# Performance work log

Hardware: AMD Instinct MI355X
Metric: run time of the kernel (lower is better)

The kernel has to match this reference:

```python
import jax, jax.numpy as jnp
import numpy as np

H_S = 1024
N_HEADS = 16
P_S = H_S // N_HEADS
LN_EPS = 1e-5


def layer_norm(x, gamma, beta):
    mu = jnp.mean(x, axis=-1, keepdims=True)
    var = jnp.var(x, axis=-1, keepdims=True)
    return (x - mu) * jax.lax.rsqrt(var + LN_EPS) * gamma + beta


def setup_inputs() -> dict:
    key = jax.random.key(0)
    ks = jax.random.split(key, 8)
    scale = 1.0 / np.sqrt(H_S)
    B, S = 4, 2048
    return {
        "q": jax.random.normal(ks[0], (B, S, H_S), jnp.float32),
        "k": jax.random.normal(ks[1], (B, S, H_S), jnp.float32),
        "v": jax.random.normal(ks[2], (B, S, H_S), jnp.float32),
        "ln_q_g": jnp.ones((H_S,), jnp.float32),
        "ln_q_b": jnp.zeros((H_S,), jnp.float32),
        "ln_k_g": jnp.ones((H_S,), jnp.float32),
        "ln_k_b": jnp.zeros((H_S,), jnp.float32),
        "ln_v_g": jnp.ones((H_S,), jnp.float32),
        "ln_v_b": jnp.zeros((H_S,), jnp.float32),
        "w_q": jax.random.normal(ks[3], (H_S, H_S), jnp.float32) * scale,
        "w_k": jax.random.normal(ks[4], (H_S, H_S), jnp.float32) * scale,
        "w_v": jax.random.normal(ks[5], (H_S, H_S), jnp.float32) * scale,
        "w_fc": jax.random.normal(ks[6], (H_S, H_S), jnp.float32) * scale,
        "b_fc": jnp.zeros((H_S,), jnp.float32),
    }


def _split_heads(x):
    # (b, s, h_s) -> (b, n_heads, s, p_s)
    b, s, _ = x.shape
    return x.reshape(b, s, N_HEADS, P_S).transpose(0, 2, 1, 3)


def reference(q, k, v, ln_q_g, ln_q_b, ln_k_g, ln_k_b, ln_v_g, ln_v_b,
              w_q, w_k, w_v, w_fc, b_fc):
    b, q_l, _ = q.shape
    # LayerNorm + Linear (bias=False) for Q/K/V, then head split
    qh = _split_heads(layer_norm(q, ln_q_g, ln_q_b) @ w_q.T)
    kh = _split_heads(layer_norm(k, ln_k_g, ln_k_b) @ w_k.T)
    vh = _split_heads(layer_norm(v, ln_v_g, ln_v_b) @ w_v.T)
    # scaled dot-product attention (clipping_distance=None path), scale 1/sqrt(p_s)
    scores = jnp.einsum("bhqp,bhkp->bhqk", qh, kh) / jnp.sqrt(jnp.float32(P_S))
    attn = jax.nn.softmax(scores, axis=-1)
    ctx = jnp.einsum("bhqk,bhkp->bhqp", attn, vh)
    # join heads: (b, h, q, p) -> (b, q, h_s)
    ctx = ctx.transpose(0, 2, 1, 3).reshape(b, q_l, H_S)
    out = ctx @ w_fc.T + b_fc
    # residual (dropout p=0.0 -> identity)
    return q + out
```

## Files before the change

kernel.cpp:

```cpp
#include <hip/hip_runtime.h>

#define HS 1024
#define NH 16
#define PS 64
#define SS 2048
#define NB 4
#define MTOT (NB * SS)
#define QSCALE 0.18033688011112042f

typedef __bf16 bf16x8 __attribute__((ext_vector_type(8)));
typedef float f32x4 __attribute__((ext_vector_type(4)));

__device__ __forceinline__ unsigned short f2bf(float f) {
  union { __bf16 h; unsigned short u; } c;
  c.h = (__bf16)f;
  return c.u;
}
__device__ __forceinline__ unsigned int pk2(float a, float b) {
  union { __bf16 h[2]; unsigned int u; } c;
  c.h[0] = (__bf16)a; c.h[1] = (__bf16)b;
  return c.u;
}
__device__ __forceinline__ float exp2x(float x) {
  float r; asm("v_exp_f32 %0, %1" : "=v"(r) : "v"(x)); return r;
}
__device__ __forceinline__ int kp32(int k) {
  return (k & ~31) | ((k & 12) << 1) | ((k & 16) >> 2) | (k & 3);
}

__device__ __forceinline__ void gload16(const void* g, void* lds) {
  __builtin_amdgcn_global_load_lds(
      (const __attribute__((address_space(1))) unsigned int*)g,
      (__attribute__((address_space(3))) unsigned int*)lds, 16, 0, 0);
}

__device__ __forceinline__ bf16x8 ldfrag128(const unsigned short* base, int r, int c) {
  union { bf16x8 v; uint4 u; } f;
  f.u = *reinterpret_cast<const uint4*>(base + r * 64 + ((c ^ (r & 7)) << 3));
  return f.v;
}

__global__ __launch_bounds__(256) void ln3_kernel(
    const float* __restrict__ x0, const float* __restrict__ x1, const float* __restrict__ x2,
    const float* __restrict__ g0, const float* __restrict__ b0,
    const float* __restrict__ g1, const float* __restrict__ b1,
    const float* __restrict__ g2, const float* __restrict__ b2,
    unsigned short* __restrict__ y0, unsigned short* __restrict__ y1,
    unsigned short* __restrict__ y2) {
  const int z = blockIdx.y;
  const float* x = z == 0 ? x0 : z == 1 ? x1 : x2;
  const float* g = z == 0 ? g0 : z == 1 ? g1 : g2;
  const float* bt = z == 0 ? b0 : z == 1 ? b1 : b2;
  unsigned short* y = z == 0 ? y0 : z == 1 ? y1 : y2;
  const int row = blockIdx.x;
  const int t = threadIdx.x;
  const float4 v = reinterpret_cast<const float4*>(x + (size_t)row * HS)[t];
  float s = v.x + v.y + v.z + v.w;
  float s2 = v.x * v.x + v.y * v.y + v.z * v.z + v.w * v.w;
#pragma unroll
  for (int m = 32; m; m >>= 1) { s += __shfl_xor(s, m); s2 += __shfl_xor(s2, m); }
  __shared__ float red[8];
  if ((t & 63) == 0) { red[t >> 6] = s; red[4 + (t >> 6)] = s2; }
  __syncthreads();
  s = red[0] + red[1] + red[2] + red[3];
  s2 = red[4] + red[5] + red[6] + red[7];
  const float mean = s * (1.0f / HS);
  const float var = s2 * (1.0f / HS) - mean * mean;
  const float rs = rsqrtf(var + 1e-5f);
  const float4 gv = reinterpret_cast<const float4*>(g)[t];
  const float4 bv = reinterpret_cast<const float4*>(bt)[t];
  uint2 o;
  o.x = pk2((v.x - mean) * rs * gv.x + bv.x, (v.y - mean) * rs * gv.y + bv.y);
  o.y = pk2((v.z - mean) * rs * gv.z + bv.z, (v.w - mean) * rs * gv.w + bv.w);
  *reinterpret_cast<uint2*>(y + (size_t)row * HS + kp32(4 * t)) = o;
}

__global__ __launch_bounds__(256) void castw_kernel(
    const float* __restrict__ w0, const float* __restrict__ w1,
    const float* __restrict__ w2, const float* __restrict__ w3,
    unsigned short* __restrict__ o0, unsigned short* __restrict__ o1,
    unsigned short* __restrict__ o2, unsigned short* __restrict__ o3) {
  const int which = blockIdx.x >> 10;
  const float* w = which == 0 ? w0 : which == 1 ? w1 : which == 2 ? w2 : w3;
  unsigned short* o = which == 0 ? o0 : which == 1 ? o1 : which == 2 ? o2 : o3;
  const int i = (blockIdx.x & 1023) * 256 + threadIdx.x;
  float4 v = reinterpret_cast<const float4*>(w)[i];
  uint2 u;
  u.x = pk2(v.x, v.y);
  u.y = pk2(v.z, v.w);
  *reinterpret_cast<uint2*>(o + (size_t)(i >> 8) * 1024 + kp32((i << 2) & 1023)) = u;
}

__global__ __launch_bounds__(512, 4) void gemm_qkv(
    const unsigned short* __restrict__ Aq, const unsigned short* __restrict__ Ak,
    const unsigned short* __restrict__ Av, const unsigned short* __restrict__ Wq,
    const unsigned short* __restrict__ Wk, const unsigned short* __restrict__ Wv,
    unsigned short* __restrict__ Pq, unsigned short* __restrict__ Pk,
    unsigned short* __restrict__ Pv, int zbase) {
  const int z = zbase + blockIdx.z;
  const unsigned short* A = z == 0 ? Aq : z == 1 ? Ak : Av;
  const unsigned short* Bw = z == 0 ? Wq : z == 1 ? Wk : Wv;
  unsigned short* out = z == 0 ? Pq : z == 1 ? Pk : Pv;
  __shared__ unsigned short As[128 * 64];
  __shared__ unsigned short Bs[128 * 64];
  const int t = threadIdx.x;
  const int id = blockIdx.x + 8 * blockIdx.y;
  const int xcd = id & 7, j = id >> 3;
  const int colT = (j & 7) * 128;
  const int rowT = (xcd * 8 + (j >> 3)) * 128;
  const int lane = t & 63;
  const int w = t >> 6;
  const int wr = (w >> 2) * 64, wc = (w & 3) * 32;
  const int c16 = lane & 15, g = lane >> 4, g4 = g << 2;
  const unsigned short* Ab = A + (size_t)rowT * 1024;
  const unsigned short* Bb = Bw + (size_t)colT * 1024;
  f32x4 acc[4][2] = {};
  for (int kt = 0; kt < 1024; kt += 64) {
#pragma unroll
    for (int i = 0; i < 2; ++i) {
      const int c = i * 512 + t;
      const int col = kt + (((c ^ (c >> 3)) & 7) << 3);
      gload16(Ab + (size_t)(c >> 3) * 1024 + col, As + c * 8);
      gload16(Bb + (size_t)(c >> 3) * 1024 + col, Bs + c * 8);
    }
    __syncthreads();
#pragma unroll
    for (int kk = 0; kk < 2; ++kk) {
      bf16x8 aF[4], bF[2];
#pragma unroll
      for (int m = 0; m < 4; ++m) aF[m] = ldfrag128(As, wr + m * 16 + c16, kk * 4 + g);
#pragma unroll
      for (int n = 0; n < 2; ++n) bF[n] = ldfrag128(Bs, wc + n * 16 + c16, kk * 4 + g);
      __builtin_amdgcn_s_setprio(1);
#pragma unroll
      for (int m = 0; m < 4; ++m)
#pragma unroll
        for (int n = 0; n < 2; ++n)
          acc[m][n] = __builtin_amdgcn_mfma_f32_16x16x32_bf16(aF[m], bF[n], acc[m][n], 0, 0, 0);
      __builtin_amdgcn_s_setprio(0);
    }
    __syncthreads();
  }
  const float sc = (z == 0) ? QSCALE : 1.0f;
#pragma unroll
  for (int m = 0; m < 4; ++m) {
#pragma unroll
    for (int n = 0; n < 2; ++n) {
#pragma unroll
      for (int r = 0; r < 4; ++r) {
        const int row = rowT + wr + m * 16 + g4 + r;
        const int col = colT + wc + n * 16 + c16;
        const float val = acc[m][n][r] * sc;
        const int b = row >> 11, s = row & 2047, h = col >> 6, p = col & 63;
        if (z == 2) {
          out[(((size_t)(b * NH + h)) * PS + p) * SS + kp32(s)] = f2bf(val);
        } else {
          out[(((size_t)(b * NH + h)) * SS + s) * PS + kp32(p)] = f2bf(val);
        }
      }
    }
  }
}

__global__ __launch_bounds__(512, 4) void gemm_fc(
    const unsigned short* __restrict__ A, const unsigned short* __restrict__ Bw,
    float* __restrict__ out, const float* __restrict__ resid,
    const float* __restrict__ bias) {
  __shared__ unsigned short As[128 * 64];
  __shared__ unsigned short Bs[128 * 64];
  const int t = threadIdx.x;
  const int id = blockIdx.x + 8 * blockIdx.y;
  const int xcd = id & 7, j = id >> 3;
  const int colT = (j & 7) * 128;
  const int rowT = (xcd * 8 + (j >> 3)) * 128;
  const int lane = t & 63;
  const int w = t >> 6;
  const int wr = (w >> 2) * 64, wc = (w & 3) * 32;
  const int c16 = lane & 15, g = lane >> 4, g4 = g << 2;
  const unsigned short* Ab = A + (size_t)rowT * 1024;
  const unsigned short* Bb = Bw + (size_t)colT * 1024;
  f32x4 acc[4][2] = {};
  for (int kt = 0; kt < 1024; kt += 64) {
#pragma unroll
    for (int i = 0; i < 2; ++i) {
      const int c = i * 512 + t;
      const int col = kt + (((c ^ (c >> 3)) & 7) << 3);
      gload16(Ab + (size_t)(c >> 3) * 1024 + col, As + c * 8);
      gload16(Bb + (size_t)(c >> 3) * 1024 + col, Bs + c * 8);
    }
    __syncthreads();
#pragma unroll
    for (int kk = 0; kk < 2; ++kk) {
      bf16x8 aF[4], bF[2];
#pragma unroll
      for (int m = 0; m < 4; ++m) aF[m] = ldfrag128(As, wr + m * 16 + c16, kk * 4 + g);
#pragma unroll
      for (int n = 0; n < 2; ++n) bF[n] = ldfrag128(Bs, wc + n * 16 + c16, kk * 4 + g);
      __builtin_amdgcn_s_setprio(1);
#pragma unroll
      for (int m = 0; m < 4; ++m)
#pragma unroll
        for (int n = 0; n < 2; ++n)
          acc[m][n] = __builtin_amdgcn_mfma_f32_16x16x32_bf16(aF[m], bF[n], acc[m][n], 0, 0, 0);
      __builtin_amdgcn_s_setprio(0);
    }
    __syncthreads();
  }
#pragma unroll
  for (int m = 0; m < 4; ++m) {
#pragma unroll
    for (int n = 0; n < 2; ++n) {
#pragma unroll
      for (int r = 0; r < 4; ++r) {
        const int row = rowT + wr + m * 16 + g4 + r;
        const int col = colT + wc + n * 16 + c16;
        out[(size_t)row * HS + col] =
            acc[m][n][r] + bias[col] + resid[(size_t)row * HS + col];
      }
    }
  }
}

__device__ __forceinline__ void stage_kv128(const unsigned short* Kb,
                                            const unsigned short* Vb, int tile,
                                            unsigned short* kd, unsigned short* vd,
                                            int t) {
#pragma unroll
  for (int i = 0; i < 2; ++i) {
    const int c = i * 512 + t;
    const int rk = c >> 3;
    const int ck = ((c ^ rk) & 7) << 3;
    gload16(Kb + (size_t)(tile * 128 + rk) * PS + ck, kd + c * 8);
    const int cc = c & 511;
    const int rv = cc >> 3;
    const int cv = ((cc ^ rv) & 7) << 3;
    gload16(Vb + (size_t)rv * SS + tile * 128 + i * 64 + cv, vd + c * 8);
  }
}

__global__ __launch_bounds__(512, 4) void attn_kernel(
    const unsigned short* __restrict__ Qp, const unsigned short* __restrict__ Kp,
    const unsigned short* __restrict__ Vtg, unsigned short* __restrict__ ctx) {
  __shared__ unsigned short Ks[2][128 * 64];
  __shared__ unsigned short Vs[2][128 * 64];
  const int t = threadIdx.x;
  const int w = t >> 6, lane = t & 63;
  const int c16 = lane & 15, g = lane >> 4, g4 = g << 2;
  const int id = blockIdx.x + 8 * blockIdx.y;
  const int xcd = id & 7, j = id >> 3;
  const int bh = xcd * 8 + (j >> 3);
  const int qbase = (j & 7) * 256 + w * 32;
  const unsigned short* Qb = Qp + (size_t)bh * SS * PS;
  const unsigned short* Kb = Kp + (size_t)bh * SS * PS;
  const unsigned short* Vb = Vtg + (size_t)bh * SS * PS;

  union { bf16x8 v; unsigned short s[8]; } ou;
#pragma unroll
  for (int i = 0; i < 8; ++i) ou.s[i] = 0x3F80;
  const bf16x8 onesv = ou.v;

  bf16x8 qF0[2], qF1[2];
#pragma unroll
  for (int kkc = 0; kkc < 2; ++kkc) {
    union { bf16x8 v; uint4 u; } f0, f1;
    f0.u = *reinterpret_cast<const uint4*>(Qb + (size_t)(qbase + c16) * PS + ((kkc * 4 + g) << 3));
    f1.u = *reinterpret_cast<const uint4*>(Qb + (size_t)(qbase + 16 + c16) * PS + ((kkc * 4 + g) << 3));
    qF0[kkc] = f0.v; qF1[kkc] = f1.v;
  }
  f32x4 o0[4] = {}, o1[4] = {};
  f32x4 ol0 = {}, ol1 = {};

  stage_kv128(Kb, Vb, 0, Ks[0], Vs[0], t);

  int buf = 0;
  for (int kt = 0; kt < 16; ++kt) {
    asm volatile("s_waitcnt vmcnt(0) lgkmcnt(0)" ::: "memory");
    __builtin_amdgcn_s_barrier();
    __builtin_amdgcn_sched_barrier(0);
    if (kt + 1 < 16) stage_kv128(Kb, Vb, kt + 1, Ks[buf ^ 1], Vs[buf ^ 1], t);

#pragma unroll
    for (int hh = 0; hh < 2; ++hh) {
      const unsigned short* kh = &Ks[buf][hh * 4096];
      const unsigned short* vh = &Vs[buf][hh * 4096];

      f32x4 s0[4] = {}, s1[4] = {};
      __builtin_amdgcn_s_setprio(1);
#pragma unroll
      for (int kkc = 0; kkc < 2; ++kkc)
#pragma unroll
        for (int nf = 0; nf < 4; ++nf) {
          const bf16x8 kf = ldfrag128(kh, nf * 16 + c16, kkc * 4 + g);
          s0[nf] = __builtin_amdgcn_mfma_f32_16x16x32_bf16(kf, qF0[kkc], s0[nf], 0, 0, 0);
          s1[nf] = __builtin_amdgcn_mfma_f32_16x16x32_bf16(kf, qF1[kkc], s1[nf], 0, 0, 0);
        }
      __builtin_amdgcn_s_setprio(0);

#pragma unroll
      for (int nf = 0; nf < 4; ++nf)
#pragma unroll
        for (int r = 0; r < 4; ++r) {
          s0[nf][r] = exp2x(s0[nf][r]);
          s1[nf][r] = exp2x(s1[nf][r]);
        }

      __builtin_amdgcn_s_setprio(1);
#pragma unroll
      for (int kkc = 0; kkc < 2; ++kkc) {
        union { bf16x8 v; unsigned int u[4]; } pa0, pa1;
        pa0.u[0] = pk2(s0[2 * kkc][0], s0[2 * kkc][1]);
        pa0.u[1] = pk2(s0[2 * kkc][2], s0[2 * kkc][3]);
        pa0.u[2] = pk2(s0[2 * kkc + 1][0], s0[2 * kkc + 1][1]);
        pa0.u[3] = pk2(s0[2 * kkc + 1][2], s0[2 * kkc + 1][3]);
        pa1.u[0] = pk2(s1[2 * kkc][0], s1[2 * kkc][1]);
        pa1.u[1] = pk2(s1[2 * kkc][2], s1[2 * kkc][3]);
        pa1.u[2] = pk2(s1[2 * kkc + 1][0], s1[2 * kkc + 1][1]);
        pa1.u[3] = pk2(s1[2 * kkc + 1][2], s1[2 * kkc + 1][3]);
        ol0 = __builtin_amdgcn_mfma_f32_16x16x32_bf16(pa0.v, onesv, ol0, 0, 0, 0);
        ol1 = __builtin_amdgcn_mfma_f32_16x16x32_bf16(pa1.v, onesv, ol1, 0, 0, 0);
#pragma unroll
        for (int pf = 0; pf < 4; ++pf) {
          const bf16x8 vf = ldfrag128(vh, pf * 16 + c16, kkc * 4 + g);
          o0[pf] = __builtin_amdgcn_mfma_f32_16x16x32_bf16(pa0.v, vf, o0[pf], 0, 0, 0);
          o1[pf] = __builtin_amdgcn_mfma_f32_16x16x32_bf16(pa1.v, vf, o1[pf], 0, 0, 0);
        }
      }
      __builtin_amdgcn_s_setprio(0);
    }

    buf ^= 1;
  }

  float i0[4], i1[4];
#pragma unroll
  for (int r = 0; r < 4; ++r) { i0[r] = 1.0f / ol0[r]; i1[r] = 1.0f / ol1[r]; }
  const int b = bh >> 4, h = bh & 15;
#pragma unroll
  for (int pf = 0; pf < 4; ++pf) {
#pragma unroll
    for (int r = 0; r < 4; ++r) {
      const int col = kp32(h * PS + pf * 16 + c16);
      const int sA = qbase + g4 + r, sB = qbase + 16 + g4 + r;
      ctx[((size_t)(b * SS + sA)) * HS + col] = f2bf(o0[pf][r] * i0[r]);
      ctx[((size_t)(b * SS + sB)) * HS + col] = f2bf(o1[pf][r] * i1[r]);
    }
  }
}

extern "C" void kernel_launch(void* const* d_in, const int* in_sizes, int n_in,
                              void* d_out, int out_size, void* d_ws, size_t ws_size,
                              hipStream_t stream) {
  const float* q = (const float*)d_in[0];
  const float* k = (const float*)d_in[1];
  const float* v = (const float*)d_in[2];
  const float* ln_q_g = (const float*)d_in[3];
  const float* ln_q_b = (const float*)d_in[4];
  const float* ln_k_g = (const float*)d_in[5];
  const float* ln_k_b = (const float*)d_in[6];
  const float* ln_v_g = (const float*)d_in[7];
  const float* ln_v_b = (const float*)d_in[8];
  const float* w_q = (const float*)d_in[9];
  const float* w_k = (const float*)d_in[10];
  const float* w_v = (const float*)d_in[11];
  const float* w_fc = (const float*)d_in[12];
  const float* b_fc = (const float*)d_in[13];

  char* ws = (char*)d_ws;
  const bool merged = ws_size >= ((size_t)104 << 20);

  if (merged) {
    unsigned short* xq = (unsigned short*)(ws);
    unsigned short* xk = (unsigned short*)(ws + (16 << 20));
    unsigned short* xv = (unsigned short*)(ws + (32 << 20));
    unsigned short* ctx = (unsigned short*)(ws);
    unsigned short* wqb = (unsigned short*)(ws + (48 << 20));
    unsigned short* wkb = (unsigned short*)(ws + (50 << 20));
    unsigned short* wvb = (unsigned short*)(ws + (52 << 20));
    unsigned short* wfcb = (unsigned short*)(ws + (54 << 20));
    unsigned short* pq = (unsigned short*)(ws + (56 << 20));
    unsigned short* pk = (unsigned short*)(ws + (72 << 20));
    unsigned short* pv = (unsigned short*)(ws + (88 << 20));

    castw_kernel<<<4096, 256, 0, stream>>>(w_q, w_k, w_v, w_fc, wqb, wkb, wvb, wfcb);
    ln3_kernel<<<dim3(MTOT, 3), 256, 0, stream>>>(q, k, v, ln_q_g, ln_q_b, ln_k_g,
                                                  ln_k_b, ln_v_g, ln_v_b, xq, xk, xv);
    gemm_qkv<<<dim3(8, 64, 3), 512, 0, stream>>>(xq, xk, xv, wqb, wkb, wvb, pq, pk, pv, 0);
    attn_kernel<<<dim3(8, 64), 512, 0, stream>>>(pq, pk, pv, ctx);
    gemm_fc<<<dim3(8, 64), 512, 0, stream>>>(ctx, wfcb, (float*)d_out, q, b_fc);
  } else {
    unsigned short* xln = (unsigned short*)(ws);
    unsigned short* ctx = (unsigned short*)(ws);
    unsigned short* wqb = (unsigned short*)(ws + (16 << 20));
    unsigned short* wkb = (unsigned short*)(ws + (18 << 20));
    unsigned short* wvb = (unsigned short*)(ws + (20 << 20));
    unsigned short* wfcb = (unsigned short*)(ws + (22 << 20));
    unsigned short* pq = (unsigned short*)(ws + (24 << 20));
    unsigned short* pk = (unsigned short*)(ws + (40 << 20));
    unsigned short* pv = (unsigned short*)(ws + (56 << 20));

    castw_kernel<<<4096, 256, 0, stream>>>(w_q, w_k, w_v, w_fc, wqb, wkb, wvb, wfcb);
    ln3_kernel<<<dim3(MTOT, 1), 256, 0, stream>>>(q, q, q, ln_q_g, ln_q_b, ln_q_g,
                                                  ln_q_b, ln_q_g, ln_q_b, xln, xln, xln);
    gemm_qkv<<<dim3(8, 64, 1), 512, 0, stream>>>(xln, xln, xln, wqb, wqb, wqb,
                                                 pq, pq, pq, 0);
    ln3_kernel<<<dim3(MTOT, 1), 256, 0, stream>>>(k, k, k, ln_k_g, ln_k_b, ln_k_g,
                                                  ln_k_b, ln_k_g, ln_k_b, xln, xln, xln);
    gemm_qkv<<<dim3(8, 64, 1), 512, 0, stream>>>(xln, xln, xln, wkb, wkb, wkb,
                                                 pk, pk, pk, 1);
    ln3_kernel<<<dim3(MTOT, 1), 256, 0, stream>>>(v, v, v, ln_v_g, ln_v_b, ln_v_g,
                                                  ln_v_b, ln_v_g, ln_v_b, xln, xln, xln);
    gemm_qkv<<<dim3(8, 64, 1), 512, 0, stream>>>(xln, xln, xln, wvb, wvb, wvb,
                                                 pv, pv, pv, 2);
    attn_kernel<<<dim3(8, 64), 512, 0, stream>>>(pq, pk, pv, ctx);
    gemm_fc<<<dim3(8, 64), 512, 0, stream>>>(ctx, wfcb, (float*)d_out, q, b_fc);
  }
}
```

Before: 201.1 us.

## Double-buffer LDS tiles in QKV and FC GEMMs to overlap loads with MFMA

Both projection GEMMs now keep two LDS buffers for the A and B tiles. The next K-tile is issued by direct global-to-LDS loads while MFMAs run on the current one, and the trailing barrier is gone, leaving one wait+barrier per iteration. This targets global-load latency that was exposed between K steps. LDS use per block doubles to 64 KB, which may lower how many blocks fit per CU compared with the launch-bounds hint of 4.

Measured after the change: 197.2 us (median of 2 runs). -2.0%, faster.

```diff
diff --git a/kernel.cpp b/kernel.cpp
--- a/kernel.cpp
+++ b/kernel.cpp
@@ -91,6 +91,18 @@
   *reinterpret_cast<uint2*>(o + (size_t)(i >> 8) * 1024 + kp32((i << 2) & 1023)) = u;
 }
 
+__device__ __forceinline__ void stage_ab(const unsigned short* Ab, const unsigned short* Bb,
+                                         int kt, unsigned short* ad, unsigned short* bd,
+                                         int t) {
+#pragma unroll
+  for (int i = 0; i < 2; ++i) {
+    const int c = i * 512 + t;
+    const int col = kt + (((c ^ (c >> 3)) & 7) << 3);
+    gload16(Ab + (size_t)(c >> 3) * 1024 + col, ad + c * 8);
+    gload16(Bb + (size_t)(c >> 3) * 1024 + col, bd + c * 8);
+  }
+}
+
 __global__ __launch_bounds__(512, 4) void gemm_qkv(
     const unsigned short* __restrict__ Aq, const unsigned short* __restrict__ Ak,
     const unsigned short* __restrict__ Av, const unsigned short* __restrict__ Wq,
@@ -101,8 +113,8 @@
   const unsigned short* A = z == 0 ? Aq : z == 1 ? Ak : Av;
   const unsigned short* Bw = z == 0 ? Wq : z == 1 ? Wk : Wv;
   unsigned short* out = z == 0 ? Pq : z == 1 ? Pk : Pv;
-  __shared__ unsigned short As[128 * 64];
-  __shared__ unsigned short Bs[128 * 64];
+  __shared__ unsigned short As[2][128 * 64];
+  __shared__ unsigned short Bs[2][128 * 64];
   const int t = threadIdx.x;
   const int id = blockIdx.x + 8 * blockIdx.y;
   const int xcd = id & 7, j = id >> 3;
@@ -115,22 +127,20 @@
   const unsigned short* Ab = A + (size_t)rowT * 1024;
   const unsigned short* Bb = Bw + (size_t)colT * 1024;
   f32x4 acc[4][2] = {};
-  for (int kt = 0; kt < 1024; kt += 64) {
-#pragma unroll
-    for (int i = 0; i < 2; ++i) {
-      const int c = i * 512 + t;
-      const int col = kt + (((c ^ (c >> 3)) & 7) << 3);
-      gload16(Ab + (size_t)(c >> 3) * 1024 + col, As + c * 8);
-      gload16(Bb + (size_t)(c >> 3) * 1024 + col, Bs + c * 8);
-    }
-    __syncthreads();
+  stage_ab(Ab, Bb, 0, As[0], Bs[0], t);
+  int buf = 0;
+  for (int kt = 0; kt < 16; ++kt) {
+    asm volatile("s_waitcnt vmcnt(0) lgkmcnt(0)" ::: "memory");
+    __builtin_amdgcn_s_barrier();
+    __builtin_amdgcn_sched_barrier(0);
+    if (kt + 1 < 16) stage_ab(Ab, Bb, (kt + 1) * 64, As[buf ^ 1], Bs[buf ^ 1], t);
 #pragma unroll
     for (int kk = 0; kk < 2; ++kk) {
       bf16x8 aF[4], bF[2];
 #pragma unroll
-      for (int m = 0; m < 4; ++m) aF[m] = ldfrag128(As, wr + m * 16 + c16, kk * 4 + g);
-#pragma unroll
-      for (int n = 0; n < 2; ++n) bF[n] = ldfrag128(Bs, wc + n * 16 + c16, kk * 4 + g);
+      for (int m = 0; m < 4; ++m) aF[m] = ldfrag128(As[buf], wr + m * 16 + c16, kk * 4 + g);
+#pragma unroll
+      for (int n = 0; n < 2; ++n) bF[n] = ldfrag128(Bs[buf], wc + n * 16 + c16, kk * 4 + g);
       __builtin_amdgcn_s_setprio(1);
 #pragma unroll
       for (int m = 0; m < 4; ++m)
@@ -139,7 +149,7 @@
           acc[m][n] = __builtin_amdgcn_mfma_f32_16x16x32_bf16(aF[m], bF[n], acc[m][n], 0, 0, 0);
       __builtin_amdgcn_s_setprio(0);
     }
-    __syncthreads();
+    buf ^= 1;
   }
   const float sc = (z == 0) ? QSCALE : 1.0f;
 #pragma unroll
@@ -166,8 +176,8 @@
     const unsigned short* __restrict__ A, const unsigned short* __restrict__ Bw,
     float* __restrict__ out, const float* __restrict__ resid,
     const float* __restrict__ bias) {
-  __shared__ unsigned short As[128 * 64];
-  __shared__ unsigned short Bs[128 * 64];
+  __shared__ unsigned short As[2][128 * 64];
+  __shared__ unsigned short Bs[2][128 * 64];
   const int t = threadIdx.x;
   const int id = blockIdx.x + 8 * blockIdx.y;
   const int xcd = id & 7, j = id >> 3;
@@ -180,22 +190,20 @@
   const unsigned short* Ab = A + (size_t)rowT * 1024;
   const unsigned short* Bb = Bw + (size_t)colT * 1024;
   f32x4 acc[4][2] = {};
-  for (int kt = 0; kt < 1024; kt += 64) {
-#pragma unroll
-    for (int i = 0; i < 2; ++i) {
-      const int c = i * 512 + t;
-      const int col = kt + (((c ^ (c >> 3)) & 7) << 3);
-      gload16(Ab + (size_t)(c >> 3) * 1024 + col, As + c * 8);
-      gload16(Bb + (size_t)(c >> 3) * 1024 + col, Bs + c * 8);
-    }
-    __syncthreads();
+  stage_ab(Ab, Bb, 0, As[0], Bs[0], t);
+  int buf = 0;
+  for (int kt = 0; kt < 16; ++kt) {
+    asm volatile("s_waitcnt vmcnt(0) lgkmcnt(0)" ::: "memory");
+    __builtin_amdgcn_s_barrier();
+    __builtin_amdgcn_sched_barrier(0);
+    if (kt + 1 < 16) stage_ab(Ab, Bb, (kt + 1) * 64, As[buf ^ 1], Bs[buf ^ 1], t);
 #pragma unroll
     for (int kk = 0; kk < 2; ++kk) {
       bf16x8 aF[4], bF[2];
 #pragma unroll
-      for (int m = 0; m < 4; ++m) aF[m] = ldfrag128(As, wr + m * 16 + c16, kk * 4 + g);
-#pragma unroll
-      for (int n = 0; n < 2; ++n) bF[n] = ldfrag128(Bs, wc + n * 16 + c16, kk * 4 + g);
+      for (int m = 0; m < 4; ++m) aF[m] = ldfrag128(As[buf], wr + m * 16 + c16, kk * 4 + g);
+#pragma unroll
+      for (int n = 0; n < 2; ++n) bF[n] = ldfrag128(Bs[buf], wc + n * 16 + c16, kk * 4 + g);
       __builtin_amdgcn_s_setprio(1);
 #pragma unroll
       for (int m = 0; m < 4; ++m)
@@ -204,7 +212,7 @@
           acc[m][n] = __builtin_amdgcn_mfma_f32_16x16x32_bf16(aF[m], bF[n], acc[m][n], 0, 0, 0);
       __builtin_amdgcn_s_setprio(0);
     }
-    __syncthreads();
+    buf ^= 1;
   }
 #pragma unroll
   for (int m = 0; m < 4; ++m) {
```
